# Performance work log

Hardware: AMD Instinct MI355X
Metric: run time of the kernel (lower is better)

## Reference

```python
import jax, jax.numpy as jnp
import numpy as np
from jax import lax

B, H, W, T, C = 2, 28, 28, 28, 192
WS = 7
NH = 6
HD = C // NH
N = WS ** 3
L = H * W * T

# static relative position index (matches torch buffer construction)
_coords = np.stack(np.meshgrid(np.arange(WS), np.arange(WS), np.arange(WS), indexing='ij'))  # (3,7,7,7)
_flat = _coords.reshape(3, -1)
_rel = (_flat[:, :, None] - _flat[:, None, :]).transpose(1, 2, 0).astype(np.int64)  # (N,N,3)
_rel[..., 0] += WS - 1; _rel[..., 1] += WS - 1; _rel[..., 2] += WS - 1
_rel[..., 0] *= (2 * WS - 1) ** 2
_rel[..., 1] *= (2 * WS - 1)
REL_IDX = jnp.asarray(_rel.sum(-1))  # (N,N)


def setup_inputs() -> dict:
    key = jax.random.key(0)
    ks = jax.random.split(key, 24)
    s = 0.02
    d = {
        'x': jax.random.normal(ks[0], (B, L, C), jnp.float32),
        'y': jax.random.normal(ks[1], (B, L, C), jnp.float32),
        'mask_matrix': jnp.zeros((64, N, N), jnp.float32),
        'norm1_g': jnp.ones((C,), jnp.float32),
        'norm1_b': jnp.zeros((C,), jnp.float32),
        'qkv_w': jax.random.normal(ks[2], (3 * C, C), jnp.float32) * s,
        'qkv_b': jnp.zeros((3 * C,), jnp.float32),
        'proj_w': jax.random.normal(ks[3], (C, C), jnp.float32) * s,
        'proj_b': jnp.zeros((C,), jnp.float32),
        'rpb_table': jax.random.normal(ks[4], ((2 * WS - 1) ** 3, NH), jnp.float32) * s,
        'norm2_g': jnp.ones((C,), jnp.float32),
        'norm2_b': jnp.zeros((C,), jnp.float32),
        'fc1_w': jax.random.normal(ks[5], (4 * C, C), jnp.float32) * s,
        'fc1_b': jnp.zeros((4 * C,), jnp.float32),
        'fc2_w': jax.random.normal(ks[6], (C, 4 * C), jnp.float32) * s,
        'fc2_b': jnp.zeros((C,), jnp.float32),
        'cab1_w': jax.random.normal(ks[7], (C // 3, C, 3, 3, 3), jnp.float32) * s,
        'cab1_b': jnp.zeros((C // 3,), jnp.float32),
        'cab2_w': jax.random.normal(ks[8], (C, C // 3, 3, 3, 3), jnp.float32) * s,
        'cab2_b': jnp.zeros((C,), jnp.float32),
        'ca1_w': jax.random.normal(ks[9], (C // 16, C), jnp.float32) * s,
        'ca1_b': jnp.zeros((C // 16,), jnp.float32),
        'ca2_w': jax.random.normal(ks[10], (C, C // 16), jnp.float32) * s,
        'ca2_b': jnp.zeros((C,), jnp.float32),
    }
    return d


def _ln(x, g, b, eps=1e-5):
    m = x.mean(-1, keepdims=True)
    v = jnp.mean(jnp.square(x - m), axis=-1, keepdims=True)
    return (x - m) * lax.rsqrt(v + eps) * g + b


def _conv3d(x, w, b, pad):
    out = lax.conv_general_dilated(x, w, (1, 1, 1), [(pad, pad)] * 3,
                                   dimension_numbers=('NCDHW', 'OIDHW', 'NCDHW'))
    return out + b[None, :, None, None, None]


def _cab(x5, cab1_w, cab1_b, cab2_w, cab2_b, ca1_w, ca1_b, ca2_w, ca2_b):
    # x5: (B,H,W,T,C) -> conv in NCDHW
    xc = x5.transpose(0, 4, 1, 2, 3)
    h = jax.nn.gelu(_conv3d(xc, cab1_w, cab1_b, 1), approximate=False)
    h = _conv3d(h, cab2_w, cab2_b, 1)
    # channel attention (adaptive avg pool to 1 + 1x1 convs)
    p = h.mean(axis=(2, 3, 4))                       # (B,C)
    a = jax.nn.relu(p @ ca1_w.T + ca1_b)
    a = jax.nn.sigmoid(a @ ca2_w.T + ca2_b)          # (B,C)
    h = h * a[:, :, None, None, None]
    return h.transpose(0, 2, 3, 4, 1).reshape(B, L, C)


def _window_partition(t):
    t = t.reshape(B, H // WS, WS, W // WS, WS, T // WS, WS, C)
    return t.transpose(0, 1, 3, 5, 2, 4, 6, 7).reshape(-1, N, C)


def _window_reverse(wins):
    t = wins.reshape(B, H // WS, W // WS, T // WS, WS, WS, WS, C)
    return t.transpose(0, 1, 4, 2, 5, 3, 6, 7).reshape(B, H, W, T, C)


def reference(x, y, mask_matrix, norm1_g, norm1_b, qkv_w, qkv_b, proj_w, proj_b,
              rpb_table, norm2_g, norm2_b, fc1_w, fc1_b, fc2_w, fc2_b,
              cab1_w, cab1_b, cab2_w, cab2_b, ca1_w, ca1_b, ca2_w, ca2_b):
    scale = HD ** (-0.5)
    shortcut = x
    xn = _ln(x, norm1_g, norm1_b)
    yn = _ln(y, norm1_g, norm1_b)
    x5 = xn.reshape(B, H, W, T, C)
    y5 = yn.reshape(B, H, W, T, C)

    conv_x = _cab(x5, cab1_w, cab1_b, cab2_w, cab2_b, ca1_w, ca1_b, ca2_w, ca2_b)

    # shift_size = (0,0,0): no roll, mask unused
    xw = _window_partition(x5)  # (B_, N, C)
    yw = _window_partition(y5)
    B_ = xw.shape[0]

    qkv_x = (xw @ qkv_w.T + qkv_b).reshape(B_, N, 3, NH, HD).transpose(2, 0, 3, 1, 4)
    qkv_y = (yw @ qkv_w.T + qkv_b).reshape(B_, N, 3, NH, HD).transpose(2, 0, 3, 1, 4)
    q = qkv_x[0] * scale          # (B_,NH,N,HD)
    k, v = qkv_y[1], qkv_y[2]

    attn = jnp.einsum('bhnd,bhmd->bhnm', q, k)
    rpb = rpb_table[REL_IDX.reshape(-1)].reshape(N, N, NH).transpose(2, 0, 1)  # (NH,N,N)
    attn = jax.nn.softmax(attn + rpb[None], axis=-1)
    out = jnp.einsum('bhnm,bhmd->bhnd', attn, v).transpose(0, 2, 1, 3).reshape(B_, N, C)
    out = out @ proj_w.T + proj_b

    attn_x = _window_reverse(out).reshape(B, L, C)

    x = shortcut + attn_x + conv_x
    h = _ln(x, norm2_g, norm2_b)
    h = jax.nn.gelu(h @ fc1_w.T + fc1_b, approximate=False) @ fc2_w.T + fc2_b
    return x + h
```

## Files before the change

kernel.cpp:

```cpp
#include <hip/hip_runtime.h>
#include <math.h>

constexpr int CB  = 2;
constexpr int CL  = 28 * 28 * 28;
constexpr int CC  = 192;
constexpr int CM  = CB * CL;

typedef unsigned short ushortT;
typedef __attribute__((ext_vector_type(8))) short bf16x8;
typedef __attribute__((ext_vector_type(4))) float f32x4;

__device__ __forceinline__ int xcd_swz(int lid, int total) {
  int q = total >> 3, r = total & 7;
  int x = lid & 7, s = lid >> 3;
  return (x < r ? x * (q + 1) : r * (q + 1) + (x - r) * q) + s;
}

__device__ __forceinline__ int tt_to_pos(int tt, int& b) {
  int bw = tt / 343;
  int n  = tt - bw * 343;
  b = bw >> 6;
  int wi = bw & 63;
  int n0 = n / 49, r = n - n0 * 49;
  int n1 = r / 7,  n2 = r - n1 * 7;
  int h = (wi >> 4) * 7 + n0;
  int w = ((wi >> 2) & 3) * 7 + n1;
  int t = (wi & 3) * 7 + n2;
  return (h * 28 + w) * 28 + t;
}

__device__ __forceinline__ float gelu_exact(float x) {
  return 0.5f * x * (1.0f + erff(x * 0.70710678118654752f));
}

__device__ __forceinline__ ushortT f2b(float x) {
  unsigned int u = __builtin_bit_cast(unsigned int, x);
  unsigned int r = (u + 0x7FFFu + ((u >> 16) & 1u)) >> 16;
  return (ushortT)r;
}
__device__ __forceinline__ float b2f(ushortT u) {
  return __builtin_bit_cast(float, (unsigned int)u << 16);
}

typedef __attribute__((address_space(3))) unsigned int lds_uint;
typedef const __attribute__((address_space(1))) unsigned int glb_uint;
__device__ __forceinline__ void stage16(const ushortT* g, ushortT* l) {
#if defined(__has_builtin) && __has_builtin(__builtin_amdgcn_global_load_lds)
  __builtin_amdgcn_global_load_lds((glb_uint*)g, (lds_uint*)l, 16, 0, 0);
#else
  *(uint4*)l = *(const uint4*)g;
#endif
}

__device__ __forceinline__ const bf16x8* ldsfrag(const ushortT* base, int row, int chunk) {
  return (const bf16x8*)((const char*)base + row * 128 + ((chunk ^ (row & 7)) << 4));
}

__global__ __launch_bounds__(256) void ln_prep_kernel(
    const float* __restrict__ in0, const float* __restrict__ in1,
    const float* __restrict__ g, const float* __restrict__ bb,
    ushortT* __restrict__ out0, ushortT* __restrict__ out1,
    const float* __restrict__ qkvw, const float* __restrict__ projw,
    const float* __restrict__ fc1w, const float* __restrict__ fc2w,
    const float* __restrict__ w1, const float* __restrict__ w2,
    const float* __restrict__ rpb,
    ushortT* qkvwb, ushortT* projwb, ushortT* fc1wb, ushortT* fc2wb,
    ushortT* w1rb, ushortT* w2rb, float4* rpb4) {
  int bid = blockIdx.x;
  if (bid < 21952) {
    int wave = threadIdx.x >> 6;
    int lane = threadIdx.x & 63;
    const float* in = (bid & 1) ? in1 : in0;
    ushortT* out = (bid & 1) ? out1 : out0;
    int row = (bid >> 1) * 4 + wave;
    const float* p = in + (size_t)row * CC;
    float v0 = p[lane], v1 = p[lane + 64], v2 = p[lane + 128];
    float s = v0 + v1 + v2;
    for (int o = 32; o; o >>= 1) s += __shfl_xor(s, o, 64);
    float mean = s * (1.0f / 192.0f);
    float d0 = v0 - mean, d1 = v1 - mean, d2 = v2 - mean;
    float qs = d0 * d0 + d1 * d1 + d2 * d2;
    for (int o = 32; o; o >>= 1) qs += __shfl_xor(qs, o, 64);
    float rs = rsqrtf(qs * (1.0f / 192.0f) + 1e-5f);
    ushortT* po = out + (size_t)row * CC;
    po[lane]       = f2b(d0 * rs * g[lane]       + bb[lane]);
    po[lane + 64]  = f2b(d1 * rs * g[lane + 64]  + bb[lane + 64]);
    po[lane + 128] = f2b(d2 * rs * g[lane + 128] + bb[lane + 128]);
    return;
  }
  int i = (bid - 21952) * 256 + threadIdx.x;
  if (i < 110592) { qkvwb[i] = f2b(qkvw[i]); return; }
  i -= 110592;
  if (i < 36864) { projwb[i] = f2b(projw[i]); return; }
  i -= 36864;
  if (i < 147456) { fc1wb[i] = f2b(fc1w[i]); return; }
  i -= 147456;
  if (i < 147456) { fc2wb[i] = f2b(fc2w[i]); return; }
  i -= 147456;
  if (i < 331776) {
    int o = i / 5184, r = i - o * 5184, tap = r / 192, c = r - tap * 192;
    w1rb[i] = f2b(w1[o * 5184 + c * 27 + tap]); return;
  }
  i -= 331776;
  if (i < 331776) {
    int o = i / 1728, r = i - o * 1728, tap = r / 64, c = r - tap * 64;
    w2rb[i] = f2b(w2[o * 1728 + c * 27 + tap]); return;
  }
  i -= 331776;
  if (i < 6 * 88 * 352) {
    int head = i / (88 * 352);
    int rem = i - head * 88 * 352;
    int qgrp = rem / 352, k = rem - qgrp * 352;
    float4 v = make_float4(0.f, 0.f, 0.f, 0.f);
    if (k < 343) {
      int b0 = k / 49, rb = k - b0 * 49; int b1 = rb / 7, b2 = rb - b1 * 7;
#pragma unroll
      for (int r = 0; r < 4; ++r) {
        int q = qgrp * 4 + r;
        if (q < 343) {
          int a0 = q / 49, ra = q - a0 * 49; int a1 = ra / 7, a2 = ra - a1 * 7;
          int ridx = ((a0 - b0 + 6) * 13 + (a1 - b1 + 6)) * 13 + (a2 - b2 + 6);
          (&v.x)[r] = rpb[ridx * 6 + head];
        }
      }
    }
    rpb4[i] = v;
  }
}

#define CORE_IDS \
  const int tid = threadIdx.x; \
  const int wave = tid >> 6, lane = tid & 63; \
  const int fr = lane & 15, g = lane >> 4; \
  const int wr = wave >> 1, wc = wave & 1;

#define ZERO_ACC(NF) \
  f32x4 acc[2][NF]; \
  _Pragma("unroll") \
  for (int m_ = 0; m_ < 2; ++m_) { \
    _Pragma("unroll") \
    for (int n_ = 0; n_ < NF; ++n_) acc[m_][n_] = (f32x4){0.f, 0.f, 0.f, 0.f}; \
  }

#define SETUP_A_ROWMAJOR(BASE, LDA, BX) \
  const ushortT* pa[2]; ushortT* la[2]; \
  _Pragma("unroll") \
  for (int i = 0; i < 2; ++i) { \
    int slot = i * 256 + tid; int row_ = slot >> 3; \
    int cc8 = ((slot & 7) ^ (row_ & 7)) * 8; \
    pa[i] = (BASE) + (size_t)((BX) * 64 + row_) * (LDA) + cc8; \
    la[i] = Asl + slot * 8; \
  }

#define SETUP_A_WINDOWED(BASE, BX) \
  const ushortT* pa[2]; ushortT* la[2]; \
  _Pragma("unroll") \
  for (int i = 0; i < 2; ++i) { \
    int slot = i * 256 + tid; int row_ = slot >> 3; \
    int cc8 = ((slot & 7) ^ (row_ & 7)) * 8; \
    int bq_; int pos_ = tt_to_pos((BX) * 64 + row_, bq_); \
    pa[i] = (BASE) + ((size_t)bq_ * CL + pos_) * CC + cc8; \
    la[i] = Asl + slot * 8; \
  }

#define SETUP_B(BASE, ROWOFF, LDB, NR) \
  const ushortT* pb[NR]; ushortT* lb[NR]; \
  _Pragma("unroll") \
  for (int i = 0; i < NR; ++i) { \
    int slot = i * 256 + tid; int row_ = slot >> 3; \
    int cc8 = ((slot & 7) ^ (row_ & 7)) * 8; \
    pb[i] = (BASE) + (size_t)((ROWOFF) + row_) * (LDB) + cc8; \
    lb[i] = Bsl + slot * 8; \
  }

#define STAGE_AB(NR) \
  _Pragma("unroll") \
  for (int i = 0; i < 2; ++i) { stage16(pa[i], la[i]); pa[i] += 64; } \
  _Pragma("unroll") \
  for (int i = 0; i < NR; ++i) { stage16(pb[i], lb[i]); pb[i] += 64; }

#define CORE_MFMA(NF) \
  __syncthreads(); \
  _Pragma("unroll") \
  for (int kk = 0; kk < 2; ++kk) { \
    bf16x8 a0 = *ldsfrag(Asl, wr * 32 + fr, kk * 4 + g); \
    bf16x8 a1 = *ldsfrag(Asl, wr * 32 + 16 + fr, kk * 4 + g); \
    _Pragma("unroll") \
    for (int n_ = 0; n_ < NF; ++n_) { \
      bf16x8 bn = *ldsfrag(Bsl, wc * ((NF) * 16) + n_ * 16 + fr, kk * 4 + g); \
      acc[0][n_] = __builtin_amdgcn_mfma_f32_16x16x32_bf16(a0, bn, acc[0][n_], 0, 0, 0); \
      acc[1][n_] = __builtin_amdgcn_mfma_f32_16x16x32_bf16(a1, bn, acc[1][n_], 0, 0, 0); \
    } \
  } \
  __syncthreads();

#define M128_ZERO \
  f32x4 acc[4][4]; \
  _Pragma("unroll") \
  for (int m_ = 0; m_ < 4; ++m_) \
    _Pragma("unroll") \
    for (int n_ = 0; n_ < 4; ++n_) acc[m_][n_] = (f32x4){0.f, 0.f, 0.f, 0.f};

#define M128_SETUP_A_ROWMAJOR(BASE, LDA) \
  const ushortT* pa[4]; ushortT* la[4]; \
  _Pragma("unroll") \
  for (int i = 0; i < 4; ++i) { \
    int slot = i * 256 + tid; int row_ = slot >> 3; \
    int cc8 = ((slot & 7) ^ (row_ & 7)) * 8; \
    pa[i] = (BASE) + (size_t)(mblk * 128 + row_) * (LDA) + cc8; \
    la[i] = Asl + slot * 8; \
  }

#define M128_SETUP_A_WINDOWED(BASE) \
  const ushortT* pa[4]; ushortT* la[4]; \
  _Pragma("unroll") \
  for (int i = 0; i < 4; ++i) { \
    int slot = i * 256 + tid; int row_ = slot >> 3; \
    int cc8 = ((slot & 7) ^ (row_ & 7)) * 8; \
    int bq_; int pos_ = tt_to_pos(mblk * 128 + row_, bq_); \
    pa[i] = (BASE) + ((size_t)bq_ * CL + pos_) * CC + cc8; \
    la[i] = Asl + slot * 8; \
  }

#define M128_SETUP_B(BASE, ROWOFF, LDB) \
  const ushortT* pb[4]; ushortT* lb[4]; \
  _Pragma("unroll") \
  for (int i = 0; i < 4; ++i) { \
    int slot = i * 256 + tid; int row_ = slot >> 3; \
    int cc8 = ((slot & 7) ^ (row_ & 7)) * 8; \
    pb[i] = (BASE) + (size_t)((ROWOFF) + row_) * (LDB) + cc8; \
    lb[i] = Bsl + slot * 8; \
  }

#define M128_STAGE \
  { _Pragma("unroll") \
    for (int i = 0; i < 4; ++i) { stage16(pa[i], la[i]); pa[i] += 64; } \
    _Pragma("unroll") \
    for (int i = 0; i < 4; ++i) { stage16(pb[i], lb[i]); pb[i] += 64; } }

#define M128_MFMA \
  { _Pragma("unroll") \
    for (int kk = 0; kk < 2; ++kk) { \
      bf16x8 am[4], bn[4]; \
      _Pragma("unroll") \
      for (int m_ = 0; m_ < 4; ++m_) am[m_] = *ldsfrag(Asl, wr * 64 + m_ * 16 + fr, kk * 4 + g); \
      _Pragma("unroll") \
      for (int n_ = 0; n_ < 4; ++n_) bn[n_] = *ldsfrag(Bsl, wc * 64 + n_ * 16 + fr, kk * 4 + g); \
      _Pragma("unroll") \
      for (int m_ = 0; m_ < 4; ++m_) \
        _Pragma("unroll") \
        for (int n_ = 0; n_ < 4; ++n_) \
          acc[m_][n_] = __builtin_amdgcn_mfma_f32_16x16x32_bf16(am[m_], bn[n_], acc[m_][n_], 0, 0, 0); \
    } }

#define M128_LOOP(KS) \
  _Pragma("unroll") \
  for (int ks = 0; ks < (KS); ++ks) { \
    M128_STAGE \
    __syncthreads(); \
    M128_MFMA \
    __syncthreads(); \
  }

__device__ __forceinline__ void gemmq_body(int bx, ushortT* Asl, ushortT* Bsl,
                                           const ushortT* __restrict__ xnb,
                                           const ushortT* __restrict__ qkvwb,
                                           const float* __restrict__ qkvb,
                                           ushortT* __restrict__ qout) {
  CORE_IDS
  ZERO_ACC(6)
  SETUP_A_WINDOWED(xnb, bx)
  SETUP_B(qkvwb, 0, 192, 6)
  for (int ks = 0; ks < 3; ++ks) {
    STAGE_AB(6)
    CORE_MFMA(6)
  }
#pragma unroll
  for (int n = 0; n < 6; ++n) {
    int jj = wc * 96 + n * 16 + fr;
    int head = jj >> 5, d = jj & 31;
    float bias = qkvb[jj];
#pragma unroll
    for (int m = 0; m < 2; ++m)
#pragma unroll
      for (int r = 0; r < 4; ++r) {
        int tt = bx * 64 + wr * 32 + m * 16 + g * 4 + r;
        int bw = tt / 343, nn = tt - bw * 343;
        qout[(((size_t)bw * 6 + head) * 343 + nn) * 32 + d] =
            f2b((acc[m][n][r] + bias) * 0.17677669529663687f);
      }
  }
}

__device__ __forceinline__ void kv_body(int bx, ushortT* Asl, ushortT* Bsl,
                                        const ushortT* __restrict__ ynb,
                                        const ushortT* __restrict__ qkvwb,
                                        const float* __restrict__ qkvb,
                                        ushortT* __restrict__ kout,
                                        ushortT* __restrict__ vout) {
  CORE_IDS
  const int wid = xcd_swz(bx, 343 * 3);
  const int mblk = wid / 3;
  const int jb = (wid - mblk * 3) * 128;
  M128_ZERO
  M128_SETUP_A_WINDOWED(ynb)
  M128_SETUP_B(qkvwb, 192 + jb, 192)
  M128_LOOP(3)
#pragma unroll
  for (int ni = 0; ni < 4; ++ni) {
    int jj = jb + wc * 64 + ni * 16 + fr;
    float bias = qkvb[192 + jj];
#pragma unroll
    for (int mi = 0; mi < 4; ++mi)
#pragma unroll
      for (int r = 0; r < 4; ++r) {
        int tt = mblk * 128 + wr * 64 + mi * 16 + g * 4 + r;
        int bw = tt / 343, nn = tt - bw * 343;
        float val = acc[mi][ni][r] + bias;
        if (jj < 192) {
          int head = jj >> 5, d = jj & 31;
          kout[(((size_t)bw * 6 + head) * 343 + nn) * 32 + d] = f2b(val);
        } else {
          int jv = jj - 192;
          int head = jv >> 5, d = jv & 31;
          vout[((size_t)bw * 6 + head) * 11264 + (size_t)d * 352 + nn] = f2b(val);
        }
      }
  }
}

template <int CIN, int COUTT, int MODE>
__device__ __forceinline__ void conv_body(int bx, ushortT* Asl, ushortT* Bsl,
                                          const ushortT* __restrict__ src,
                                          const ushortT* __restrict__ wrw,
                                          const float* __restrict__ bias,
                                          void* __restrict__ dst,
                                          float* __restrict__ part) {
  constexpr int KT = 27 * CIN;
  constexpr int KN = KT / 64;
  constexpr int NY = (MODE == 2) ? 4 : (COUTT / 64);
  constexpr int NBLK = 343 * NY;
  const int tid = threadIdx.x;
  const int wave = tid >> 6, lane = tid & 63;
  const int fr = lane & 15, g = lane >> 4;
  const int wid = xcd_swz(bx, NBLK);
  const int mblk = wid / NY;
  const int ysub = wid - mblk * NY;
  f32x4 acc[2][4];
#pragma unroll
  for (int m = 0; m < 2; ++m)
#pragma unroll
    for (int n = 0; n < 4; ++n) acc[m][n] = (f32x4){0.f, 0.f, 0.f, 0.f};

  const int kb = (MODE == 2) ? (ysub * KN) / 4 : 0;
  const int ke = (MODE == 2) ? ((ysub + 1) * KN) / 4 : KN;
  const int jbN = (MODE == 0) ? ysub * 64 : 0;

  const ushortT* srcb[4];
  ushortT* la[4];
  unsigned vmask[4];
#pragma unroll
  for (int i = 0; i < 4; ++i) {
    int slot = i * 256 + tid; int row_ = slot >> 3;
    int cc8 = ((slot & 7) ^ (row_ & 7)) * 8;
    int grow = mblk * 128 + row_;
    int bbq = grow / CL;
    int pos = grow - bbq * CL;
    int h = pos / 784, w = (pos / 28) % 28, t = pos % 28;
    unsigned vm = 0;
#pragma unroll
    for (int tap = 0; tap < 27; ++tap) {
      int dh = tap / 9 - 1, dw = (tap / 3) % 3 - 1, dt = tap % 3 - 1;
      bool ok = ((unsigned)(h + dh) < 28u) && ((unsigned)(w + dw) < 28u) &&
                ((unsigned)(t + dt) < 28u);
      vm |= (unsigned)ok << tap;
    }
    vmask[i] = vm;
    srcb[i] = src + ((size_t)bbq * CL + pos) * CIN + cc8;
    la[i] = Asl + slot * 8;
  }
  const ushortT* pb[2]; ushortT* lb[2];
#pragma unroll
  for (int i = 0; i < 2; ++i) {
    int slot = i * 256 + tid; int row_ = slot >> 3;
    int cc8 = ((slot & 7) ^ (row_ & 7)) * 8;
    pb[i] = wrw + (size_t)(jbN + row_) * KT + kb * 64 + cc8;
    lb[i] = Bsl + slot * 8;
  }

  auto loadA = [&](int ks, int i) -> uint4 {
    int tap, cb;
    if (CIN == 64) { tap = ks; cb = 0; }
    else           { tap = ks / 3; cb = (ks - tap * 3) * 64; }
    int off = ((tap / 9 - 1) * 784 + ((tap / 3) % 3 - 1) * 28 + (tap % 3 - 1)) * CIN + cb;
    uint4 v = make_uint4(0u, 0u, 0u, 0u);
    if ((vmask[i] >> tap) & 1u) v = *(const uint4*)(srcb[i] + off);
    return v;
  };

  uint4 vr[4];
#pragma unroll
  for (int i = 0; i < 4; ++i) vr[i] = loadA(kb, i);
  for (int ks = kb; ks < ke; ++ks) {
#pragma unroll
    for (int i = 0; i < 4; ++i) *(uint4*)la[i] = vr[i];
#pragma unroll
    for (int i = 0; i < 2; ++i) { stage16(pb[i], lb[i]); pb[i] += 64; }
    __syncthreads();
    bool more = (ks + 1 < ke);
    if (more) {
#pragma unroll
      for (int i = 0; i < 4; ++i) vr[i] = loadA(ks + 1, i);
    }
#pragma unroll
    for (int kk = 0; kk < 2; ++kk) {
      bf16x8 a0 = *ldsfrag(Asl, wave * 32 + fr, kk * 4 + g);
      bf16x8 a1 = *ldsfrag(Asl, wave * 32 + 16 + fr, kk * 4 + g);
#pragma unroll
      for (int n = 0; n < 4; ++n) {
        bf16x8 bn = *ldsfrag(Bsl, n * 16 + fr, kk * 4 + g);
        acc[0][n] = __builtin_amdgcn_mfma_f32_16x16x32_bf16(a0, bn, acc[0][n], 0, 0, 0);
        acc[1][n] = __builtin_amdgcn_mfma_f32_16x16x32_bf16(a1, bn, acc[1][n], 0, 0, 0);
      }
    }
    __syncthreads();
  }
  if (MODE == 2) {
#pragma unroll
    for (int n = 0; n < 4; ++n) {
      int jj = n * 16 + fr;
#pragma unroll
      for (int m = 0; m < 2; ++m)
#pragma unroll
        for (int r = 0; r < 4; ++r) {
          int grow = mblk * 128 + wave * 32 + m * 16 + g * 4 + r;
          ((float*)dst)[((size_t)ysub * CM + grow) * 64 + jj] = acc[m][n][r];
        }
    }
  } else {
    float* red = (float*)Asl;
#pragma unroll
    for (int n = 0; n < 4; ++n) {
      int jj = n * 16 + fr;
      float bs = bias[jbN + jj];
      float s0 = 0.f, s1 = 0.f;
#pragma unroll
      for (int m = 0; m < 2; ++m)
#pragma unroll
        for (int r = 0; r < 4; ++r) {
          int grow = mblk * 128 + wave * 32 + m * 16 + g * 4 + r;
          float v = acc[m][n][r] + bs;
          ((ushortT*)dst)[(size_t)grow * COUTT + jbN + jj] = f2b(v);
          if (grow < CL) s0 += v; else s1 += v;
        }
      s0 += __shfl_xor(s0, 16, 64); s0 += __shfl_xor(s0, 32, 64);
      s1 += __shfl_xor(s1, 16, 64); s1 += __shfl_xor(s1, 32, 64);
      if (g == 0) {
        red[((wave * 4 + n) * 16 + fr) * 2 + 0] = s0;
        red[((wave * 4 + n) * 16 + fr) * 2 + 1] = s1;
      }
    }
    __syncthreads();
    if (tid < 128) {
      int chl = tid >> 1, bsel = tid & 1;
      float s = 0.f;
#pragma unroll
      for (int wv = 0; wv < 4; ++wv)
        s += red[((wv * 4 + (chl >> 4)) * 16 + (chl & 15)) * 2 + bsel];
      if (s != 0.0f) atomicAdd(&part[bsel * 192 + jbN + chl], s);
    }
  }
}

constexpr int KP  = 36;
constexpr int VP  = 356;
constexpr int VP2 = 200;

__device__ __forceinline__ void attn_body(int bx, ushortT* Kl, ushortT* Vt, ushortT* Pl,
                                          const ushortT* __restrict__ qb,
                                          const ushortT* __restrict__ kb,
                                          const ushortT* __restrict__ vb,
                                          const float* __restrict__ rpb4,
                                          ushortT* __restrict__ aout) {
  const int tid = threadIdx.x;
  const int wave = tid >> 6, lane = tid & 63;
  const int fr = lane & 15, g = lane >> 4, fk = g * 8;
  const int wid = xcd_swz(bx, 768 * 2);
  const int wh = wid >> 1;
  const int qhalf = wid & 1;
  const int bw = wh / 6, head = wh - bw * 6;
  const ushortT* kp = kb + (size_t)wh * 343 * 32;
  const ushortT* vp = vb + (size_t)wh * 11264;
  const ushortT* qp = qb + (size_t)wh * 343 * 32;
  const f32x4* bp4 = (const f32x4*)rpb4 + (size_t)head * 88 * 352;

  for (int c = tid; c < 1372; c += 256) {
    int key = c >> 2, pp = c & 3;
    *(uint4*)&Kl[key * KP + pp * 8] = *(const uint4*)(kp + (size_t)c * 8);
  }
  for (int c = tid; c < 1408; c += 256) {
    int d = c / 44, p = c - d * 44;
    *(uint4*)&Vt[d * VP + p * 8] = *(const uint4*)(vp + (size_t)c * 8);
  }
  __syncthreads();

  for (int qi = 0; qi < 3; ++qi) {
    const int q0 = (qhalf * 3 + qi) * 64;

    int qrow = q0 + wave * 16 + fr; if (qrow > 342) qrow = 342;
    bf16x8 aq = *(const bf16x8*)(qp + (size_t)qrow * 32 + fk);

    const int qgrp = (q0 + wave * 16) / 4 + g;
    f32x4 sc[22];
#pragma unroll
    for (int t = 0; t < 22; ++t) {
      f32x4 cini = bp4[(size_t)qgrp * 352 + t * 16 + fr];
      bf16x8 bk = *(const bf16x8*)&Kl[(t * 16 + fr) * KP + fk];
      sc[t] = __builtin_amdgcn_mfma_f32_16x16x32_bf16(aq, bk, cini, 0, 0, 0);
    }
    if (fr > 6) { sc[21][0] = -1e30f; sc[21][1] = -1e30f; sc[21][2] = -1e30f; sc[21][3] = -1e30f; }

    float rinv[4];
#pragma unroll
    for (int r = 0; r < 4; ++r) {
      float sum = 0.0f;
#pragma unroll
      for (int t = 0; t < 22; ++t) {
        float e = __expf(sc[t][r]);
        sc[t][r] = e;
        sum += e;
      }
      sum += __shfl_xor(sum, 1, 64); sum += __shfl_xor(sum, 2, 64);
      sum += __shfl_xor(sum, 4, 64); sum += __shfl_xor(sum, 8, 64);
      rinv[r] = 1.0f / sum;
    }

    f32x4 o0 = {0.f, 0.f, 0.f, 0.f}, o1 = {0.f, 0.f, 0.f, 0.f};

#pragma unroll
    for (int t = 0; t < 12; ++t)
#pragma unroll
      for (int r = 0; r < 4; ++r)
        Pl[(wave * 16 + g * 4 + r) * VP2 + t * 16 + fr] = f2b(sc[t][r]);
    asm volatile("s_waitcnt lgkmcnt(0)" ::: "memory");
#pragma unroll
    for (int s = 0; s < 6; ++s) {
      bf16x8 ap  = *(const bf16x8*)&Pl[(wave * 16 + fr) * VP2 + s * 32 + fk];
      bf16x8 bv0 = *(const bf16x8*)&Vt[fr * VP + s * 32 + fk];
      bf16x8 bv1 = *(const bf16x8*)&Vt[(16 + fr) * VP + s * 32 + fk];
      o0 = __builtin_amdgcn_mfma_f32_16x16x32_bf16(ap, bv0, o0, 0, 0, 0);
      o1 = __builtin_amdgcn_mfma_f32_16x16x32_bf16(ap, bv1, o1, 0, 0, 0);
    }
    asm volatile("s_waitcnt lgkmcnt(0)" ::: "memory");

#pragma unroll
    for (int t = 12; t < 22; ++t)
#pragma unroll
      for (int r = 0; r < 4; ++r)
        Pl[(wave * 16 + g * 4 + r) * VP2 + (t - 12) * 16 + fr] = f2b(sc[t][r]);
    asm volatile("s_waitcnt lgkmcnt(0)" ::: "memory");
#pragma unroll
    for (int s = 0; s < 5; ++s) {
      bf16x8 ap  = *(const bf16x8*)&Pl[(wave * 16 + fr) * VP2 + s * 32 + fk];
      bf16x8 bv0 = *(const bf16x8*)&Vt[fr * VP + 192 + s * 32 + fk];
      bf16x8 bv1 = *(const bf16x8*)&Vt[(16 + fr) * VP + 192 + s * 32 + fk];
      o0 = __builtin_amdgcn_mfma_f32_16x16x32_bf16(ap, bv0, o0, 0, 0, 0);
      o1 = __builtin_amdgcn_mfma_f32_16x16x32_bf16(ap, bv1, o1, 0, 0, 0);
    }
    asm volatile("s_waitcnt lgkmcnt(0)" ::: "memory");

#pragma unroll
    for (int r = 0; r < 4; ++r) {
      int q = q0 + wave * 16 + g * 4 + r;
      if (q < 343) {
        float ri = rinv[r];
        size_t base = ((size_t)bw * 343 + q) * 192 + head * 32;
        aout[base + fr]      = f2b(o0[r] * ri);
        aout[base + 16 + fr] = f2b(o1[r] * ri);
      }
    }
  }
}

__global__ __launch_bounds__(256) void phaseA(const ushortT* __restrict__ xnb,
                                              const ushortT* __restrict__ ynb,
                                              const ushortT* __restrict__ qkvwb,
                                              const float* __restrict__ qkvb,
                                              const ushortT* __restrict__ w1rb,
                                              ushortT* __restrict__ qout,
                                              ushortT* __restrict__ kout,
                                              ushortT* __restrict__ vout,
                                              float* __restrict__ pc1) {
  __shared__ alignas(16) ushortT SH[16384];
  const int bid = blockIdx.x;
  if (bid < 1372) {
    conv_body<192, 64, 2>(bid, SH, SH + 8192, xnb, w1rb, nullptr, pc1, nullptr);
  } else if (bid < 2401) {
    kv_body(bid - 1372, SH, SH + 8192, ynb, qkvwb, qkvb, kout, vout);
  } else {
    gemmq_body(bid - 2401, SH, SH + 4096, xnb, qkvwb, qkvb, qout);
  }
}

__global__ __launch_bounds__(256) void comb1_kernel(const float* __restrict__ pc,
                                                    const float* __restrict__ b1,
                                                    ushortT* __restrict__ h1b) {
  size_t idx = ((size_t)blockIdx.x * 256 + threadIdx.x) * 4;
  float4 a = *(const float4*)(pc + idx);
  float4 b = *(const float4*)(pc + (size_t)CM * 64 + idx);
  float4 c = *(const float4*)(pc + (size_t)CM * 128 + idx);
  float4 d = *(const float4*)(pc + (size_t)CM * 192 + idx);
  int c0 = (int)(idx & 63);
  ushortT o0 = f2b(gelu_exact(a.x + b.x + c.x + d.x + b1[c0 + 0]));
  ushortT o1 = f2b(gelu_exact(a.y + b.y + c.y + d.y + b1[c0 + 1]));
  ushortT o2 = f2b(gelu_exact(a.z + b.z + c.z + d.z + b1[c0 + 2]));
  ushortT o3 = f2b(gelu_exact(a.w + b.w + c.w + d.w + b1[c0 + 3]));
  unsigned int w0 = (unsigned int)o0 | ((unsigned int)o1 << 16);
  unsigned int w1 = (unsigned int)o2 | ((unsigned int)o3 << 16);
  *(uint2*)&h1b[idx] = make_uint2(w0, w1);
}

__global__ __launch_bounds__(256) void conv2attn(const ushortT* __restrict__ h1b,
                                                 const ushortT* __restrict__ w2rb,
                                                 const float* __restrict__ b2,
                                                 ushortT* __restrict__ h2b,
                                                 float* __restrict__ part,
                                                 const ushortT* __restrict__ qb,
                                                 const ushortT* __restrict__ kb,
                                                 const ushortT* __restrict__ vb,
                                                 const float* __restrict__ rpb4,
                                                 ushortT* __restrict__ aout) {
  __shared__ alignas(16) ushortT SH[36864];
  const int bid = blockIdx.x;
  if (bid < 1029) {
    conv_body<64, 192, 0>(bid, SH, SH + 8192, h1b, w2rb, b2, h2b, part);
  } else {
    attn_body(bid - 1029, SH, SH + 12672, SH + 24064, qb, kb, vb, rpb4, aout);
  }
}

__global__ __launch_bounds__(192) void ca_kernel(const float* __restrict__ part,
                                                 const float* __restrict__ ca1w,
                                                 const float* __restrict__ ca1b,
                                                 const float* __restrict__ ca2w,
                                                 const float* __restrict__ ca2b,
                                                 float* __restrict__ av) {
  __shared__ float pl[192];
  __shared__ float hid[12];
  int c = threadIdx.x, b = blockIdx.x;
  pl[c] = part[b * 192 + c] * (1.0f / (float)CL);
  __syncthreads();
  if (c < 12) {
    float t = ca1b[c];
    for (int i = 0; i < 192; ++i) t += ca1w[c * 192 + i] * pl[i];
    hid[c] = fmaxf(t, 0.0f);
  }
  __syncthreads();
  float t = ca2b[c];
#pragma unroll
  for (int j = 0; j < 12; ++j) t += ca2w[c * 12 + j] * hid[j];
  av[b * 192 + c] = 1.0f / (1.0f + __expf(-t));
}

__global__ __launch_bounds__(256) void proj_ln(const ushortT* __restrict__ attnrb,
                                               const ushortT* __restrict__ projwb,
                                               const float* __restrict__ projb,
                                               const float* __restrict__ x0,
                                               const ushortT* __restrict__ h2b,
                                               const float* __restrict__ cav,
                                               const float* __restrict__ n2g,
                                               const float* __restrict__ n2b,
                                               float* __restrict__ xout,
                                               ushortT* __restrict__ hlnb) {
  __shared__ alignas(16) ushortT Asl[64 * 64];
  __shared__ alignas(16) ushortT Bsl[192 * 64];
  CORE_IDS
  const int bx = blockIdx.x;
  ZERO_ACC(6)
  SETUP_A_ROWMAJOR(attnrb, CC, bx)
  SETUP_B(projwb, 0, 192, 6)
  for (int ks = 0; ks < 3; ++ks) {
    STAGE_AB(6)
    CORE_MFMA(6)
  }
  size_t sbase[2][4];
#pragma unroll
  for (int m = 0; m < 2; ++m)
#pragma unroll
    for (int r = 0; r < 4; ++r) {
      int tt = bx * 64 + wr * 32 + m * 16 + g * 4 + r;
      int bq_;
      int pos_ = tt_to_pos(tt, bq_);
      size_t base = ((size_t)bq_ * CL + pos_) * CC;
      sbase[m][r] = base;
#pragma unroll
      for (int n = 0; n < 6; ++n) {
        int jj = wc * 96 + n * 16 + fr;
        size_t addr = base + jj;
        float v = x0[addr] + acc[m][n][r] + projb[jj] + b2f(h2b[addr]) * cav[bq_ * 192 + jj];
        acc[m][n][r] = v;
        xout[addr] = v;
      }
    }
  float* stats = (float*)Asl;
#pragma unroll
  for (int m = 0; m < 2; ++m)
#pragma unroll
    for (int r = 0; r < 4; ++r) {
      float ps = 0.f, ps2 = 0.f;
#pragma unroll
      for (int n = 0; n < 6; ++n) { float v = acc[m][n][r]; ps += v; ps2 += v * v; }
      ps  += __shfl_xor(ps, 1, 64);  ps2 += __shfl_xor(ps2, 1, 64);
      ps  += __shfl_xor(ps, 2, 64);  ps2 += __shfl_xor(ps2, 2, 64);
      ps  += __shfl_xor(ps, 4, 64);  ps2 += __shfl_xor(ps2, 4, 64);
      ps  += __shfl_xor(ps, 8, 64);  ps2 += __shfl_xor(ps2, 8, 64);
      if (fr == 0) {
        int lrow = wr * 32 + m * 16 + g * 4 + r;
        stats[lrow * 4 + wc * 2]     = ps;
        stats[lrow * 4 + wc * 2 + 1] = ps2;
      }
    }
  __syncthreads();
#pragma unroll
  for (int m = 0; m < 2; ++m)
#pragma unroll
    for (int r = 0; r < 4; ++r) {
      int lrow = wr * 32 + m * 16 + g * 4 + r;
      float s  = stats[lrow * 4]     + stats[lrow * 4 + 2];
      float s2 = stats[lrow * 4 + 1] + stats[lrow * 4 + 3];
      float mean = s * (1.0f / 192.0f);
      float var  = s2 * (1.0f / 192.0f) - mean * mean;
      float rs = rsqrtf(var + 1e-5f);
      ushortT* po = hlnb + sbase[m][r];
#pragma unroll
      for (int n = 0; n < 6; ++n) {
        int jj = wc * 96 + n * 16 + fr;
        po[jj] = f2b((acc[m][n][r] - mean) * rs * n2g[jj] + n2b[jj]);
      }
    }
}

__global__ __launch_bounds__(256) void fc1_128(const ushortT* __restrict__ hlnb,
                                               const ushortT* __restrict__ fc1wb,
                                               const float* __restrict__ fc1b,
                                               ushortT* __restrict__ hidb) {
  __shared__ alignas(16) ushortT Asl[8192];
  __shared__ alignas(16) ushortT Bsl[8192];
  CORE_IDS
  const int wid = xcd_swz(blockIdx.x, 343 * 6);
  const int mblk = wid / 6;
  const int jb = (wid - mblk * 6) * 128;
  M128_ZERO
  M128_SETUP_A_ROWMAJOR(hlnb, CC)
  M128_SETUP_B(fc1wb, jb, 192)
  M128_LOOP(3)
#pragma unroll
  for (int ni = 0; ni < 4; ++ni) {
    int jj = jb + wc * 64 + ni * 16 + fr;
    float bs = fc1b[jj];
#pragma unroll
    for (int mi = 0; mi < 4; ++mi)
#pragma unroll
      for (int r = 0; r < 4; ++r) {
        int grow = mblk * 128 + wr * 64 + mi * 16 + g * 4 + r;
        hidb[(size_t)grow * 768 + jj] = f2b(gelu_exact(acc[mi][ni][r] + bs));
      }
  }
}

__global__ __launch_bounds__(256) void fc2_n(const ushortT* __restrict__ hidb,
                                             const ushortT* __restrict__ fc2wb,
                                             const float* __restrict__ fc2b,
                                             const float* __restrict__ xout,
                                             float* __restrict__ out) {
  __shared__ alignas(16) ushortT Asl[64 * 64];
  __shared__ alignas(16) ushortT Bsl[192 * 64];
  CORE_IDS
  const int bx = blockIdx.x;
  ZERO_ACC(6)
  SETUP_A_ROWMAJOR(hidb, 768, bx)
  SETUP_B(fc2wb, 0, 768, 6)
  for (int ks = 0; ks < 12; ++ks) {
    STAGE_AB(6)
    CORE_MFMA(6)
  }
#pragma unroll
  for (int n = 0; n < 6; ++n) {
    int jj = wc * 96 + n * 16 + fr;
    float bs = fc2b[jj];
#pragma unroll
    for (int m = 0; m < 2; ++m)
#pragma unroll
      for (int r = 0; r < 4; ++r) {
        int grow = bx * 64 + wr * 32 + m * 16 + g * 4 + r;
        size_t addr = (size_t)grow * CC + jj;
        out[addr] = xout[addr] + acc[m][n][r] + bs;
      }
  }
}

extern "C" void kernel_launch(void* const* d_in, const int* in_sizes, int n_in,
                              void* d_out, int out_size, void* d_ws, size_t ws_size,
                              hipStream_t stream) {
  const float* x     = (const float*)d_in[0];
  const float* y     = (const float*)d_in[1];
  const float* n1g   = (const float*)d_in[3];
  const float* n1b   = (const float*)d_in[4];
  const float* qkvw  = (const float*)d_in[5];
  const float* qkvb  = (const float*)d_in[6];
  const float* projw = (const float*)d_in[7];
  const float* projb = (const float*)d_in[8];
  const float* rpb   = (const float*)d_in[9];
  const float* n2g   = (const float*)d_in[10];
  const float* n2b   = (const float*)d_in[11];
  const float* fc1w  = (const float*)d_in[12];
  const float* fc1b  = (const float*)d_in[13];
  const float* fc2w  = (const float*)d_in[14];
  const float* fc2b  = (const float*)d_in[15];
  const float* w1    = (const float*)d_in[16];
  const float* b1    = (const float*)d_in[17];
  const float* w2    = (const float*)d_in[18];
  const float* b2    = (const float*)d_in[19];
  const float* ca1w  = (const float*)d_in[20];
  const float* ca1b  = (const float*)d_in[21];
  const float* ca2w  = (const float*)d_in[22];
  const float* ca2b  = (const float*)d_in[23];

  char* W = (char*)d_ws;
  float* out = (float*)d_out;

  ushortT* xnb  = (ushortT*)(W + 0);
  ushortT* ynb  = (ushortT*)(W + 16859136);
  ushortT* qbb  = (ushortT*)(W + 33718272);
  ushortT* kbb  = (ushortT*)(W + 50577408);
  ushortT* vbb  = (ushortT*)(W + 67436544);
  ushortT* h1b  = (ushortT*)(W + 84738048);
  ushortT* h2b  = (ushortT*)(W + 90357760);
  float*   xo   = (float*)(W + 124076032);
  char*    SM   = W + 157794304;
  ushortT* qkvwb  = (ushortT*)(SM);
  ushortT* projwb = (ushortT*)(SM + 221184);
  ushortT* fc1wb  = (ushortT*)(SM + 294912);
  ushortT* fc2wb  = (ushortT*)(SM + 589824);
  ushortT* w1rb   = (ushortT*)(SM + 884736);
  ushortT* w2rb   = (ushortT*)(SM + 1548288);
  float*   rpb4   = (float*)(SM + 2211840);
  float*   av     = (float*)(SM + 5185536);
  float*   part   = (float*)(SM + 5187072);
  float*   pc1    = (float*)(SM + 5319168);
  ushortT* attnrb = xnb;
  ushortT* hlnb   = ynb;
  ushortT* hidb   = (ushortT*)(W + 33718272);

  hipMemsetAsync(part, 0, 2 * 192 * sizeof(float), stream);

  ln_prep_kernel<<<21952 + 5046, 256, 0, stream>>>(
      x, y, n1g, n1b, xnb, ynb,
      qkvw, projw, fc1w, fc2w, w1, w2, rpb,
      qkvwb, projwb, fc1wb, fc2wb, w1rb, w2rb, (float4*)rpb4);

  phaseA<<<1372 + 1029 + 686, 256, 0, stream>>>(xnb, ynb, qkvwb, qkvb, w1rb,
                                                qbb, kbb, vbb, pc1);

  comb1_kernel<<<2744, 256, 0, stream>>>(pc1, b1, h1b);

  conv2attn<<<1029 + 1536, 256, 0, stream>>>(h1b, w2rb, b2, h2b, part,
                                             qbb, kbb, vbb, rpb4, attnrb);

  ca_kernel<<<2, 192, 0, stream>>>(part, ca1w, ca1b, ca2w, ca2b, av);

  proj_ln<<<686, 256, 0, stream>>>(attnrb, projwb, projb, x, h2b, av, n2g, n2b, xo, hlnb);

  fc1_128<<<343 * 6, 256, 0, stream>>>(hlnb, fc1wb, fc1b, hidb);
  fc2_n<<<686, 256, 0, stream>>>(hidb, fc2wb, fc2b, xo, out);
}
```

Measured before the change: 465.5 us.

## Split conv2 from attention kernel and fuse channel-attention into attention launch

Conv2 gets its own kernel with a smaller shared-memory footprint instead of sharing the 72KB buffer sized for attention. The attention kernel gains two extra blocks that compute the channel-attention squeeze/excite vector, which removes the separate tiny ca launch. The aim is higher conv2 occupancy without adding a launch. The cost is that conv2 and attention blocks no longer overlap within one grid.

```diff
diff --git a/kernel.cpp b/kernel.cpp
--- a/kernel.cpp
+++ b/kernel.cpp
@@ -620,46 +620,50 @@
   *(uint2*)&h1b[idx] = make_uint2(w0, w1);
 }
 
-__global__ __launch_bounds__(256) void conv2attn(const ushortT* __restrict__ h1b,
-                                                 const ushortT* __restrict__ w2rb,
-                                                 const float* __restrict__ b2,
-                                                 ushortT* __restrict__ h2b,
-                                                 float* __restrict__ part,
-                                                 const ushortT* __restrict__ qb,
-                                                 const ushortT* __restrict__ kb,
-                                                 const ushortT* __restrict__ vb,
-                                                 const float* __restrict__ rpb4,
-                                                 ushortT* __restrict__ aout) {
+__global__ __launch_bounds__(256) void conv2_kernel(const ushortT* __restrict__ h1b,
+                                                    const ushortT* __restrict__ w2rb,
+                                                    const float* __restrict__ b2,
+                                                    ushortT* __restrict__ h2b,
+                                                    float* __restrict__ part) {
+  __shared__ alignas(16) ushortT Asl[8192];
+  __shared__ alignas(16) ushortT Bsl[4096];
+  conv_body<64, 192, 0>(blockIdx.x, Asl, Bsl, h1b, w2rb, b2, h2b, part);
+}
+
+__global__ __launch_bounds__(256) void attn_ca(const ushortT* __restrict__ qb,
+                                               const ushortT* __restrict__ kb,
+                                               const ushortT* __restrict__ vb,
+                                               const float* __restrict__ rpb4,
+                                               ushortT* __restrict__ aout,
+                                               const float* __restrict__ part,
+                                               const float* __restrict__ ca1w,
+                                               const float* __restrict__ ca1b,
+                                               const float* __restrict__ ca2w,
+                                               const float* __restrict__ ca2b,
+                                               float* __restrict__ av) {
   __shared__ alignas(16) ushortT SH[36864];
-  const int bid = blockIdx.x;
-  if (bid < 1029) {
-    conv_body<64, 192, 0>(bid, SH, SH + 8192, h1b, w2rb, b2, h2b, part);
-  } else {
-    attn_body(bid - 1029, SH, SH + 12672, SH + 24064, qb, kb, vb, rpb4, aout);
-  }
-}
-
-__global__ __launch_bounds__(192) void ca_kernel(const float* __restrict__ part,
-                                                 const float* __restrict__ ca1w,
-                                                 const float* __restrict__ ca1b,
-                                                 const float* __restrict__ ca2w,
-                                                 const float* __restrict__ ca2b,
-                                                 float* __restrict__ av) {
-  __shared__ float pl[192];
-  __shared__ float hid[12];
-  int c = threadIdx.x, b = blockIdx.x;
-  pl[c] = part[b * 192 + c] * (1.0f / (float)CL);
-  __syncthreads();
-  if (c < 12) {
-    float t = ca1b[c];
-    for (int i = 0; i < 192; ++i) t += ca1w[c * 192 + i] * pl[i];
-    hid[c] = fmaxf(t, 0.0f);
-  }
-  __syncthreads();
-  float t = ca2b[c];
-#pragma unroll
-  for (int j = 0; j < 12; ++j) t += ca2w[c * 12 + j] * hid[j];
-  av[b * 192 + c] = 1.0f / (1.0f + __expf(-t));
+  const int tid = threadIdx.x;
+  if (blockIdx.x >= 1536) {
+    int b = blockIdx.x - 1536;
+    float* pl = (float*)SH;
+    float* hid = pl + 192;
+    if (tid < 192) pl[tid] = part[b * 192 + tid] * (1.0f / (float)CL);
+    __syncthreads();
+    if (tid < 12) {
+      float t = ca1b[tid];
+      for (int i = 0; i < 192; ++i) t += ca1w[tid * 192 + i] * pl[i];
+      hid[tid] = fmaxf(t, 0.0f);
+    }
+    __syncthreads();
+    if (tid < 192) {
+      float t = ca2b[tid];
+#pragma unroll
+      for (int j = 0; j < 12; ++j) t += ca2w[tid * 12 + j] * hid[j];
+      av[b * 192 + tid] = 1.0f / (1.0f + __expf(-t));
+    }
+    return;
+  }
+  attn_body(blockIdx.x, SH, SH + 12672, SH + 24064, qb, kb, vb, rpb4, aout);
 }
 
 __global__ __launch_bounds__(256) void proj_ln(const ushortT* __restrict__ attnrb,
@@ -864,10 +868,10 @@
 
   comb1_kernel<<<2744, 256, 0, stream>>>(pc1, b1, h1b);
 
-  conv2attn<<<1029 + 1536, 256, 0, stream>>>(h1b, w2rb, b2, h2b, part,
-                                             qbb, kbb, vbb, rpb4, attnrb);
-
-  ca_kernel<<<2, 192, 0, stream>>>(part, ca1w, ca1b, ca2w, ca2b, av);
+  conv2_kernel<<<1029, 256, 0, stream>>>(h1b, w2rb, b2, h2b, part);
+
+  attn_ca<<<1538, 256, 0, stream>>>(qbb, kbb, vbb, rpb4, attnrb,
+                                    part, ca1w, ca1b, ca2w, ca2b, av);
 
   proj_ln<<<686, 256, 0, stream>>>(attnrb, projwb, projb, x, h2b, av, n2g, n2b, xo, hlnb);
 
```

Result: no change. 457.8 us (-1.7%).
